# Performance work log

Hardware: AMD Instinct MI355X
Metric: run time of the kernel (lower is better)

The kernel has to match this reference:

```python
import jax, jax.numpy as jnp
import numpy as np

B, S, E, H = 2, 2048, 1024, 16
DK = E // H


def setup_inputs() -> dict:
    key = jax.random.key(0)
    ks = jax.random.split(key, 10)
    x = jax.random.normal(ks[0], (B, S, E), dtype=jnp.float32)
    mask = jax.random.randint(ks[1], (B, S, S), 0, 2).astype(bool)
    scale = 1.0 / np.sqrt(E)
    def lin(k):
        kw, kb = jax.random.split(k)
        W = jax.random.uniform(kw, (E, E), minval=-scale, maxval=scale, dtype=jnp.float32)
        b = jax.random.uniform(kb, (E,), minval=-scale, maxval=scale, dtype=jnp.float32)
        return W, b
    Wq, bq = lin(ks[2])
    Wk, bk = lin(ks[3])
    Wv, bv = lin(ks[4])
    Wo, bo = lin(ks[5])
    return {"x": x, "mask": mask, "Wq": Wq, "bq": bq, "Wk": Wk, "bk": bk,
            "Wv": Wv, "bv": bv, "Wo": Wo, "bo": bo}


def reference(x, mask, Wq, bq, Wk, bk, Wv, bv, Wo, bo):
    # projections (torch Linear: y = x @ W.T + b)
    q = x @ Wq.T + bq
    k = x @ Wk.T + bk
    v = x @ Wv.T + bv
    # separate heads: [B,S,E] -> [B,H,S,DK]
    def split(t):
        return t.reshape(B, S, H, DK).transpose(0, 2, 1, 3)
    q, k, v = split(q), split(k), split(v)
    scores = jnp.einsum("bhqd,bhkd->bhqk", q, k) / jnp.sqrt(jnp.float32(DK))
    # masked_fill: positions where mask is True get -1e9 (mask broadcast over heads)
    scores = jnp.where(mask[:, None, :, :], jnp.float32(-1e9), scores)
    attn = jax.nn.softmax(scores, axis=-1)  # dropout is identity in eval
    out = jnp.einsum("bhqk,bhkd->bhqd", attn, v)
    out = out.transpose(0, 2, 1, 3).reshape(B, S, E)  # combine heads
    return out @ Wo.T + bo
```

## Files before the change

### kernel.cpp

```cpp
#include <hip/hip_runtime.h>
#include <hip/hip_bf16.h>


typedef __attribute__((ext_vector_type(8))) short short8;
typedef __attribute__((ext_vector_type(4))) float f32x4;

#define MFMA16(a, b, c) __builtin_amdgcn_mfma_f32_16x16x32_bf16(a, b, c, 0, 0, 0)

#define BATCH 2
#define SEQ   2048
#define EMB   1024
#define HEADS 16
#define DKK   64
#define MROWS (BATCH * SEQ)

typedef __hip_bfloat16 bf16;
typedef unsigned long long u64;

static __device__ __forceinline__ short bf16b(float f) {
    union { bf16 h; short s; } u;
    u.h = __float2bfloat16(f);
    return u.s;
}
static __device__ __forceinline__ short8 ld8k(const bf16* p) {
    return *(const short8*)p;
}
static __device__ __forceinline__ short8 ld8kf(const float* p) {
    const f32x4 a = *(const f32x4*)p;
    const f32x4 b = *(const f32x4*)(p + 4);
    short8 r;
    r[0] = bf16b(a[0]); r[1] = bf16b(a[1]); r[2] = bf16b(a[2]); r[3] = bf16b(a[3]);
    r[4] = bf16b(b[0]); r[5] = bf16b(b[1]); r[6] = bf16b(b[2]); r[7] = bf16b(b[3]);
    return r;
}

static __device__ __forceinline__ void glds16(const bf16* g, bf16* l) {
    __builtin_amdgcn_global_load_lds(
        (const __attribute__((address_space(1))) void*)g,
        (__attribute__((address_space(3))) void*)l, 16, 0, 0);
}

__global__ void detect_kernel(const unsigned int* __restrict__ mw,
                              int* __restrict__ flags) {
    __shared__ int mbyte;
    if (threadIdx.x == 0) mbyte = 0;
    __syncthreads();
    int mb = 0;
    for (int i = threadIdx.x; i < 4096; i += 256)
        if (mw[i] > 1u) mb = 1;
    if (mb) atomicOr(&mbyte, 1);
    __syncthreads();
    if (threadIdx.x == 0) { flags[0] = 1; flags[1] = mbyte; }
}

__global__ __launch_bounds__(256) void pack_mask(
        const void* __restrict__ mp, u64* __restrict__ bm,
        const int* __restrict__ flags) {
    const bool m8 = flags[1] != 0;
    const unsigned char* p8 = (const unsigned char*)mp;
    const int* p32 = (const int*)mp;
    const int lane = threadIdx.x & 63;
    const int w = (blockIdx.x * 256 + threadIdx.x) >> 6;
#pragma unroll 4
    for (int i = 0; i < 32; ++i) {
        const int L = i * 4096 + w;
        const size_t e = (size_t)L * 64 + lane;
        const bool v = m8 ? (p8[e] != 0) : (p32[e] != 0);
        const u64 bal = __ballot(v);
        if (lane == 0) {
            const int qg = L >> 5, it = L & 31;
            bm[((qg >> 11) * 32 + it) * 2048 + (qg & 2047)] = bal;
        }
    }
}

__global__ __launch_bounds__(256) void cvt_all(
        const float* __restrict__ x,  const float* __restrict__ wq,
        const float* __restrict__ wk, const float* __restrict__ wv,
        const float* __restrict__ wo,
        bf16* __restrict__ xb,  bf16* __restrict__ wqb,
        bf16* __restrict__ wkb, bf16* __restrict__ wvb,
        bf16* __restrict__ wob) {
    const int bid = blockIdx.x;
    const float* s; bf16* d; int base;
    if (bid < 2048)      { s = x;  d = xb;  base = bid; }
    else if (bid < 2560) { s = wq; d = wqb; base = bid - 2048; }
    else if (bid < 3072) { s = wk; d = wkb; base = bid - 2560; }
    else if (bid < 3584) { s = wv; d = wvb; base = bid - 3072; }
    else                 { s = wo; d = wob; base = bid - 3584; }
    const int i = (base * 256 + threadIdx.x) * 8;
    *(short8*)(d + i) = ld8kf(s + i);
}

__global__ __launch_bounds__(256) void gemm_qkv_staged(
        const bf16* __restrict__ X,
        const bf16* __restrict__ Wq, const bf16* __restrict__ Wk,
        const bf16* __restrict__ Wv,
        const float* __restrict__ bq, const float* __restrict__ bk,
        const float* __restrict__ bv,
        bf16* __restrict__ qo, bf16* __restrict__ ko, bf16* __restrict__ vo) {
    __shared__ bf16 As[2][128 * 32];
    __shared__ bf16 Bs[2][128 * 32];

    const int t = threadIdx.x, lane = t & 63;
    const int wv = t >> 6;
    const int mb = blockIdx.x / 24, nb = blockIdx.x % 24;
    const int m0 = mb * 128;
    const int n0g = nb * 128;
    const int sel = n0g >> 10;
    const int n0 = n0g & 1023;
    const bf16* W     = sel == 0 ? Wq : (sel == 1 ? Wk : Wv);
    const float* bias = sel == 0 ? bq : (sel == 1 ? bk : bv);
    bf16* out         = sel == 0 ? qo : (sel == 1 ? ko : vo);

    const int wr = wv >> 1, wc = wv & 1;
    const int m_off = wr * 64, n_off = wc * 64;
    const int l16 = lane & 15, quad = lane >> 4;

    int srow[2], sg[2];
#pragma unroll
    for (int i = 0; i < 2; ++i) {
        const int c = i * 256 + t;
        srow[i] = c >> 2;
        sg[i]   = (c & 3) ^ (srow[i] & 3);
    }

    f32x4 acc[4][4];
#pragma unroll
    for (int i = 0; i < 4; ++i)
#pragma unroll
        for (int j = 0; j < 4; ++j)
            acc[i][j] = (f32x4){0.f, 0.f, 0.f, 0.f};

#pragma unroll
    for (int i = 0; i < 2; ++i) {
        glds16(X + (m0 + srow[i]) * 1024 + sg[i] * 8, &As[0][(i * 256 + t) * 8]);
        glds16(W + (n0 + srow[i]) * 1024 + sg[i] * 8, &Bs[0][(i * 256 + t) * 8]);
    }

    for (int it = 0; it < 32; ++it) {
        __syncthreads();
        if (it < 31) {
            const int ktn = (it + 1) * 32;
            const int nb_ = (it + 1) & 1;
#pragma unroll
            for (int i = 0; i < 2; ++i) {
                glds16(X + (m0 + srow[i]) * 1024 + ktn + sg[i] * 8,
                       &As[nb_][(i * 256 + t) * 8]);
                glds16(W + (n0 + srow[i]) * 1024 + ktn + sg[i] * 8,
                       &Bs[nb_][(i * 256 + t) * 8]);
            }
        }
        const bf16* Ab = As[it & 1];
        const bf16* Bb = Bs[it & 1];
        short8 af[4], bfr[4];
#pragma unroll
        for (int ii = 0; ii < 4; ++ii) {
            const int row = m_off + ii * 16 + l16;
            const int slot = quad ^ (row & 3);
            af[ii] = *(const short8*)(Ab + row * 32 + slot * 8);
        }
#pragma unroll
        for (int jj = 0; jj < 4; ++jj) {
            const int row = n_off + jj * 16 + l16;
            const int slot = quad ^ (row & 3);
            bfr[jj] = *(const short8*)(Bb + row * 32 + slot * 8);
        }
#pragma unroll
        for (int ii = 0; ii < 4; ++ii)
#pragma unroll
            for (int jj = 0; jj < 4; ++jj)
                acc[ii][jj] = MFMA16(af[ii], bfr[jj], acc[ii][jj]);
    }

#pragma unroll
    for (int j = 0; j < 4; ++j) {
        const int nl = n0 + n_off + j * 16 + l16;
        const float bj = bias[nl];
        const int h = nl >> 6, d = nl & 63;
#pragma unroll
        for (int i = 0; i < 4; ++i) {
#pragma unroll
            for (int r = 0; r < 4; ++r) {
                const int m = m0 + m_off + i * 16 + quad * 4 + r;
                const float v = acc[i][j][r] + bj;
                const int bb = m >> 11, ss = m & 2047;
                const int idx = (sel == 2)
                    ? ((bb * HEADS + h) * DKK + d) * SEQ + ss
                    : ((bb * HEADS + h) * SEQ + ss) * DKK + d;
                out[idx] = __float2bfloat16(v);
            }
        }
    }
}

__global__ __launch_bounds__(256) void gemm_out_staged(
        const bf16* __restrict__ X,
        const bf16* __restrict__ W, const float* __restrict__ bias,
        float* __restrict__ out) {
    __shared__ bf16 As[2][128 * 32];
    __shared__ bf16 Bs[2][64 * 32];

    const int t = threadIdx.x, lane = t & 63;
    const int wv = t >> 6;
    const int mb = blockIdx.x >> 4, nb = blockIdx.x & 15;
    const int m0 = mb * 128, n0 = nb * 64;
    const int wr = wv >> 1, wc = wv & 1;
    const int m_off = wr * 64, n_off = wc * 32;
    const int l16 = lane & 15, quad = lane >> 4;

    int srow[2], sg[2];
#pragma unroll
    for (int i = 0; i < 2; ++i) {
        const int c = i * 256 + t;
        srow[i] = c >> 2;
        sg[i]   = (c & 3) ^ (srow[i] & 3);
    }
    const int brow = t >> 2;
    const int bslot = (t & 3) ^ (brow & 3);

    f32x4 acc[4][2];
#pragma unroll
    for (int i = 0; i < 4; ++i)
#pragma unroll
        for (int j = 0; j < 2; ++j)
            acc[i][j] = (f32x4){0.f, 0.f, 0.f, 0.f};

#pragma unroll
    for (int i = 0; i < 2; ++i)
        glds16(X + (m0 + srow[i]) * 1024 + sg[i] * 8, &As[0][(i * 256 + t) * 8]);
    glds16(W + (n0 + brow) * 1024 + bslot * 8, &Bs[0][t * 8]);

    for (int it = 0; it < 32; ++it) {
        __syncthreads();
        if (it < 31) {
            const int ktn = (it + 1) * 32;
            const int nb_ = (it + 1) & 1;
#pragma unroll
            for (int i = 0; i < 2; ++i)
                glds16(X + (m0 + srow[i]) * 1024 + ktn + sg[i] * 8,
                       &As[nb_][(i * 256 + t) * 8]);
            glds16(W + (n0 + brow) * 1024 + ktn + bslot * 8, &Bs[nb_][t * 8]);
        }
        const bf16* Ab = As[it & 1];
        const bf16* Bb = Bs[it & 1];
        short8 af[4], bfr[2];
#pragma unroll
        for (int ii = 0; ii < 4; ++ii) {
            const int row = m_off + ii * 16 + l16;
            const int slot = quad ^ (row & 3);
            af[ii] = *(const short8*)(Ab + row * 32 + slot * 8);
        }
#pragma unroll
        for (int jj = 0; jj < 2; ++jj) {
            const int row = n_off + jj * 16 + l16;
            const int slot = quad ^ (row & 3);
            bfr[jj] = *(const short8*)(Bb + row * 32 + slot * 8);
        }
#pragma unroll
        for (int ii = 0; ii < 4; ++ii)
#pragma unroll
            for (int jj = 0; jj < 2; ++jj)
                acc[ii][jj] = MFMA16(af[ii], bfr[jj], acc[ii][jj]);
    }

#pragma unroll
    for (int j = 0; j < 2; ++j) {
        const int n = n0 + n_off + j * 16 + l16;
        const float bj = bias[n];
#pragma unroll
        for (int i = 0; i < 4; ++i) {
#pragma unroll
            for (int r = 0; r < 4; ++r) {
                const int m = m0 + m_off + i * 16 + quad * 4 + r;
                out[m * 1024 + n] = acc[i][j][r] + bj;
            }
        }
    }
}

__global__ __launch_bounds__(256, 2) void attn_kernel(
        const bf16* __restrict__ Qw,
        const bf16* __restrict__ Kw,
        const bf16* __restrict__ Vw,
        const u64* __restrict__ bmT,
        bf16* __restrict__ attn_out) {
    const int t = threadIdx.x;
    const int lane = t & 63;
    const int wv   = t >> 6;
    const int l16 = lane & 15, quad = lane >> 4;
    const int h = blockIdx.y, b = blockIdx.z;
    const int bh = b * HEADS + h;
    const int qb0 = blockIdx.x * 128;

    const bf16* Q  = Qw + bh * SEQ * DKK;
    const bf16* Kp = Kw + bh * SEQ * DKK;
    const bf16* Vt = Vw + bh * DKK * SEQ;

    __shared__ bf16 Ks[2][4096];
    __shared__ bf16 Vs[2][4096];
    __shared__ bf16 lds_p[4][2][16][72];

    short8 qf[2][2];
#pragma unroll
    for (int i = 0; i < 2; ++i)
#pragma unroll
        for (int t2 = 0; t2 < 2; ++t2)
            qf[i][t2] = ld8k(Q + (qb0 + wv * 32 + i * 16 + l16) * DKK + t2 * 32 + quad * 8);

    f32x4 o[2][4];
#pragma unroll
    for (int i = 0; i < 2; ++i)
#pragma unroll
        for (int jd = 0; jd < 4; ++jd) o[i][jd] = (f32x4){0.f, 0.f, 0.f, 0.f};
    float lsum[2][4] = {{0.f,0.f,0.f,0.f},{0.f,0.f,0.f,0.f}};

    int srow[2], sg[2];
#pragma unroll
    for (int i = 0; i < 2; ++i) {
        const int c = i * 256 + t;
        srow[i] = c >> 3;
        sg[i]   = (c & 7) ^ (srow[i] & 7);
    }

#pragma unroll
    for (int i = 0; i < 2; ++i)
        glds16(Kp + srow[i] * DKK + sg[i] * 8, &Ks[0][(i * 256 + t) * 8]);
#pragma unroll
    for (int i = 0; i < 2; ++i)
        glds16(Vt + srow[i] * SEQ + sg[i] * 8, &Vs[0][(i * 256 + t) * 8]);

    const int qrow_base = qb0 + wv * 32 + quad * 4;
    u64 mc[2][4];
#pragma unroll
    for (int i = 0; i < 2; ++i)
#pragma unroll
        for (int r = 0; r < 4; ++r)
            mc[i][r] = bmT[(size_t)(b * 32) * 2048 + qrow_base + i * 16 + r];

    const float SC = 0.18033688011f;

    for (int it = 0; it < SEQ / 64; ++it) {
        __syncthreads();
        const int nb_ = (it + 1) & 1;
        if (it < SEQ / 64 - 1) {
            const int ktn = (it + 1) * 64;
#pragma unroll
            for (int i = 0; i < 2; ++i)
                glds16(Kp + (ktn + srow[i]) * DKK + sg[i] * 8, &Ks[nb_][(i * 256 + t) * 8]);
#pragma unroll
            for (int i = 0; i < 2; ++i)
                glds16(Vt + srow[i] * SEQ + ktn + sg[i] * 8, &Vs[nb_][(i * 256 + t) * 8]);
        }
        u64 mn[2][4];
        if (it < SEQ / 64 - 1) {
#pragma unroll
            for (int i = 0; i < 2; ++i)
#pragma unroll
                for (int r = 0; r < 4; ++r)
                    mn[i][r] = bmT[(size_t)(b * 32 + it + 1) * 2048 + qrow_base + i * 16 + r];
        }

        const bf16* Kb = Ks[it & 1];
        const bf16* Vb = Vs[it & 1];

        short8 kf[2][4];
#pragma unroll
        for (int t2 = 0; t2 < 2; ++t2)
#pragma unroll
            for (int j = 0; j < 4; ++j) {
                const int row = j * 16 + l16;
                const int slot = (t2 * 4 + quad) ^ (row & 7);
                kf[t2][j] = *(const short8*)(Kb + row * 64 + slot * 8);
            }

        f32x4 s[2][4];
#pragma unroll
        for (int i = 0; i < 2; ++i)
#pragma unroll
            for (int j = 0; j < 4; ++j) {
                s[i][j] = (f32x4){0.f, 0.f, 0.f, 0.f};
#pragma unroll
                for (int t2 = 0; t2 < 2; ++t2)
                    s[i][j] = MFMA16(qf[i][t2], kf[t2][j], s[i][j]);
            }

#pragma unroll
        for (int i = 0; i < 2; ++i)
#pragma unroll
            for (int r = 0; r < 4; ++r) {
                const unsigned wlo = ~(unsigned)mc[i][r];
                const unsigned whi = ~(unsigned)(mc[i][r] >> 32);
#pragma unroll
                for (int j = 0; j < 4; ++j) {
                    const unsigned word = (j < 2) ? wlo : whi;
                    const float bitf = (float)((word >> ((j & 1) * 16 + l16)) & 1u);
                    const float p = __builtin_exp2f(s[i][j][r] * SC) * bitf;
                    lsum[i][r] += p;
                    lds_p[wv][i][quad * 4 + r][j * 16 + l16] = __float2bfloat16(p);
                }
            }

#pragma unroll
        for (int t2 = 0; t2 < 2; ++t2) {
            short8 vf[4];
#pragma unroll
            for (int jd = 0; jd < 4; ++jd) {
                const int row = jd * 16 + l16;
                const int slot = (t2 * 4 + quad) ^ (row & 7);
                vf[jd] = *(const short8*)(Vb + row * 64 + slot * 8);
            }
#pragma unroll
            for (int i = 0; i < 2; ++i) {
                short8 pf = *(const short8*)(&lds_p[wv][i][l16][t2 * 32 + quad * 8]);
#pragma unroll
                for (int jd = 0; jd < 4; ++jd)
                    o[i][jd] = MFMA16(pf, vf[jd], o[i][jd]);
            }
        }
        if (it < SEQ / 64 - 1) {
#pragma unroll
            for (int i = 0; i < 2; ++i)
#pragma unroll
                for (int r = 0; r < 4; ++r) mc[i][r] = mn[i][r];
        }
    }

#pragma unroll
    for (int i = 0; i < 2; ++i)
#pragma unroll
        for (int r = 0; r < 4; ++r) {
            float l = lsum[i][r];
#pragma unroll
            for (int off = 8; off >= 1; off >>= 1)
                l += __shfl_xor(l, off, 16);
            const float inv = 1.0f / l;
            const int q = qb0 + wv * 32 + i * 16 + quad * 4 + r;
#pragma unroll
            for (int jd = 0; jd < 4; ++jd)
                attn_out[(b * SEQ + q) * EMB + h * DKK + jd * 16 + l16] =
                    __float2bfloat16(o[i][jd][r] * inv);
        }
}

extern "C" void kernel_launch(void* const* d_in, const int* in_sizes, int n_in,
                              void* d_out, int out_size, void* d_ws, size_t ws_size,
                              hipStream_t stream) {
    char* ws = (char*)d_ws;
    const size_t MB = 1024 * 1024;
    int*  flags = (int*)ws;
    u64*  bm    = (u64*)(ws + 256);
    bf16* xb    = (bf16*)(ws + 256 + MB);
    bf16* wqb   = (bf16*)(ws + 256 + 9 * MB);
    bf16* wkb   = (bf16*)(ws + 256 + 11 * MB);
    bf16* wvb   = (bf16*)(ws + 256 + 13 * MB);
    bf16* wob   = (bf16*)(ws + 256 + 15 * MB);
    bf16* k_ws  = (bf16*)(ws + 256 + 17 * MB);
    bf16* attn_ws = xb;

    bf16* q_ws = (bf16*)d_out;
    bf16* v_ws = (bf16*)d_out + 4194304;

    detect_kernel<<<1, 256, 0, stream>>>((const unsigned int*)d_in[1], flags);
    pack_mask<<<1024, 256, 0, stream>>>(d_in[1], bm, flags);

    cvt_all<<<4096, 256, 0, stream>>>(
        (const float*)d_in[0], (const float*)d_in[2], (const float*)d_in[4],
        (const float*)d_in[6], (const float*)d_in[8],
        xb, wqb, wkb, wvb, wob);

    gemm_qkv_staged<<<768, 256, 0, stream>>>(
        xb, wqb, wkb, wvb,
        (const float*)d_in[3], (const float*)d_in[5], (const float*)d_in[7],
        q_ws, k_ws, v_ws);

    attn_kernel<<<dim3(SEQ / 128, HEADS, BATCH), 256, 0, stream>>>(
        q_ws, k_ws, v_ws, bm, attn_ws);

    gemm_out_staged<<<512, 256, 0, stream>>>(
        attn_ws, wob, (const float*)d_in[9], (float*)d_out);
}
```

Measured before the change: 278.1 us.

## Transpose score MFMA, fold softmax scale into Q, pack P stores

Folds the softmax scale (1/sqrt(dk)·log2e) into the Q projection epilogue, so the attention loop no longer multiplies scores by it. Swaps the MFMA operands so each lane holds one query row's scores, which cuts mask loads per lane from eight to two and lets P be written to LDS as packed 4-element vectors. Masking becomes an FMA bias of -1000 before exp2 instead of a multiply by a bit. Row-sum reductions move to cross-quad shuffles at the end. A masked score is then exp2(s-1000) rather than exactly zero, which is a small numerical difference from the reference.

```diff
diff --git a/kernel.cpp b/kernel.cpp
--- a/kernel.cpp
+++ b/kernel.cpp
@@ -3,6 +3,7 @@
 
 
 typedef __attribute__((ext_vector_type(8))) short short8;
+typedef __attribute__((ext_vector_type(4))) short s16x4;
 typedef __attribute__((ext_vector_type(4))) float f32x4;
 
 #define MFMA16(a, b, c) __builtin_amdgcn_mfma_f32_16x16x32_bf16(a, b, c, 0, 0, 0)
@@ -112,6 +113,7 @@
     const bf16* W     = sel == 0 ? Wq : (sel == 1 ? Wk : Wv);
     const float* bias = sel == 0 ? bq : (sel == 1 ? bk : bv);
     bf16* out         = sel == 0 ? qo : (sel == 1 ? ko : vo);
+    const float oscale = sel == 0 ? 0.18033688011f : 1.0f;
 
     const int wr = wv >> 1, wc = wv & 1;
     const int m_off = wr * 64, n_off = wc * 64;
@@ -183,7 +185,7 @@
 #pragma unroll
             for (int r = 0; r < 4; ++r) {
                 const int m = m0 + m_off + i * 16 + quad * 4 + r;
-                const float v = acc[i][j][r] + bj;
+                const float v = (acc[i][j][r] + bj) * oscale;
                 const int bb = m >> 11, ss = m & 2047;
                 const int idx = (sel == 2)
                     ? ((bb * HEADS + h) * DKK + d) * SEQ + ss
@@ -313,7 +315,7 @@
     for (int i = 0; i < 2; ++i)
 #pragma unroll
         for (int jd = 0; jd < 4; ++jd) o[i][jd] = (f32x4){0.f, 0.f, 0.f, 0.f};
-    float lsum[2][4] = {{0.f,0.f,0.f,0.f},{0.f,0.f,0.f,0.f}};
+    float lsum[2] = {0.f, 0.f};
 
     int srow[2], sg[2];
 #pragma unroll
@@ -330,15 +332,11 @@
     for (int i = 0; i < 2; ++i)
         glds16(Vt + srow[i] * SEQ + sg[i] * 8, &Vs[0][(i * 256 + t) * 8]);
 
-    const int qrow_base = qb0 + wv * 32 + quad * 4;
-    u64 mc[2][4];
-#pragma unroll
-    for (int i = 0; i < 2; ++i)
-#pragma unroll
-        for (int r = 0; r < 4; ++r)
-            mc[i][r] = bmT[(size_t)(b * 32) * 2048 + qrow_base + i * 16 + r];
-
-    const float SC = 0.18033688011f;
+    const int qlane0 = qb0 + wv * 32 + l16;
+    u64 mc[2];
+#pragma unroll
+    for (int i = 0; i < 2; ++i)
+        mc[i] = bmT[(size_t)(b * 32) * 2048 + qlane0 + i * 16];
 
     for (int it = 0; it < SEQ / 64; ++it) {
         __syncthreads();
@@ -352,13 +350,11 @@
             for (int i = 0; i < 2; ++i)
                 glds16(Vt + srow[i] * SEQ + ktn + sg[i] * 8, &Vs[nb_][(i * 256 + t) * 8]);
         }
-        u64 mn[2][4];
+        u64 mn[2];
         if (it < SEQ / 64 - 1) {
 #pragma unroll
             for (int i = 0; i < 2; ++i)
-#pragma unroll
-                for (int r = 0; r < 4; ++r)
-                    mn[i][r] = bmT[(size_t)(b * 32 + it + 1) * 2048 + qrow_base + i * 16 + r];
+                mn[i] = bmT[(size_t)(b * 32 + it + 1) * 2048 + qlane0 + i * 16];
         }
 
         const bf16* Kb = Ks[it & 1];
@@ -382,24 +378,31 @@
                 s[i][j] = (f32x4){0.f, 0.f, 0.f, 0.f};
 #pragma unroll
                 for (int t2 = 0; t2 < 2; ++t2)
-                    s[i][j] = MFMA16(qf[i][t2], kf[t2][j], s[i][j]);
-            }
-
-#pragma unroll
-        for (int i = 0; i < 2; ++i)
-#pragma unroll
-            for (int r = 0; r < 4; ++r) {
-                const unsigned wlo = ~(unsigned)mc[i][r];
-                const unsigned whi = ~(unsigned)(mc[i][r] >> 32);
-#pragma unroll
-                for (int j = 0; j < 4; ++j) {
-                    const unsigned word = (j < 2) ? wlo : whi;
-                    const float bitf = (float)((word >> ((j & 1) * 16 + l16)) & 1u);
-                    const float p = __builtin_exp2f(s[i][j][r] * SC) * bitf;
-                    lsum[i][r] += p;
-                    lds_p[wv][i][quad * 4 + r][j * 16 + l16] = __float2bfloat16(p);
+                    s[i][j] = MFMA16(kf[t2][j], qf[i][t2], s[i][j]);
+            }
+
+#pragma unroll
+        for (int i = 0; i < 2; ++i) {
+            const unsigned wlo = (unsigned)mc[i];
+            const unsigned whi = (unsigned)(mc[i] >> 32);
+#pragma unroll
+            for (int j = 0; j < 4; ++j) {
+                const unsigned half = (j < 2) ? wlo : whi;
+                const int bp0 = (j & 1) * 16 + quad * 4;
+                float p[4];
+#pragma unroll
+                for (int r = 0; r < 4; ++r) {
+                    const float bit = (float)((half >> (bp0 + r)) & 1u);
+                    const float p_ = __builtin_exp2f(__builtin_fmaf(bit, -1000.f, s[i][j][r]));
+                    p[r] = p_;
+                    lsum[i] += p_;
                 }
-            }
+                s16x4 pk;
+                pk[0] = bf16b(p[0]); pk[1] = bf16b(p[1]);
+                pk[2] = bf16b(p[2]); pk[3] = bf16b(p[3]);
+                *(s16x4*)(&lds_p[wv][i][l16][j * 16 + quad * 4]) = pk;
+            }
+        }
 
 #pragma unroll
         for (int t2 = 0; t2 < 2; ++t2) {
@@ -420,21 +423,22 @@
         }
         if (it < SEQ / 64 - 1) {
 #pragma unroll
-            for (int i = 0; i < 2; ++i)
-#pragma unroll
-                for (int r = 0; r < 4; ++r) mc[i][r] = mn[i][r];
-        }
-    }
-
+            for (int i = 0; i < 2; ++i) mc[i] = mn[i];
+        }
+    }
+
+#pragma unroll
+    for (int i = 0; i < 2; ++i) {
+        float l = lsum[i];
+        l += __shfl_xor(l, 16, 64);
+        l += __shfl_xor(l, 32, 64);
+        lsum[i] = l;
+    }
 #pragma unroll
     for (int i = 0; i < 2; ++i)
 #pragma unroll
         for (int r = 0; r < 4; ++r) {
-            float l = lsum[i][r];
-#pragma unroll
-            for (int off = 8; off >= 1; off >>= 1)
-                l += __shfl_xor(l, off, 16);
-            const float inv = 1.0f / l;
+            const float inv = 1.0f / __shfl(lsum[i], quad * 4 + r, 64);
             const int q = qb0 + wv * 32 + i * 16 + quad * 4 + r;
 #pragma unroll
             for (int jd = 0; jd < 4; ++jd)
```

Measured after the change: 268.1 us. -3.6%, faster.
